# Kernel optimization log

Hardware: AMD Instinct MI355X
Metric: run time of the kernel (lower is better)

The kernel has to match this reference:

```python
import jax, jax.numpy as jnp
import numpy as np

M0, M1 = 16, 8          # scalar / vector multiplicities (16x0e + 8x1o)
NB = 16                  # number_of_basis
RMAX = 8.0               # max_radius
N_NODES, N_EDGES = 10000, 160000
WNUM = M0*M0 + M0*M1 + M1*M1 + M1*M0  # 576, tp weight_numel


def sus(t):
    """e3nn soft_unit_step: exp(-1/t) for t>0 else 0."""
    safe = jnp.where(t > 0, t, 1.0)
    return jnp.where(t > 0, jnp.exp(-1.0 / safe), 0.0)


def setup_inputs():
    key = jax.random.key(0)
    ks = jax.random.split(key, 12)
    D = M0 + 3 * M1  # 40
    x = jax.random.normal(ks[0], (N_NODES, D), jnp.float32)
    edge_index = jax.random.randint(ks[1], (2, N_EDGES), 0, N_NODES, jnp.int32)
    edge_attr = jax.random.normal(ks[2], (N_EDGES, 4), jnp.float32)  # sh lmax=1
    node_attr = jnp.ones((N_NODES, 1), jnp.float32)
    batch = jnp.zeros((N_NODES,), jnp.int32)
    amf = jax.random.uniform(ks[3], (N_EDGES, 1), jnp.float32) * RMAX  # edge lengths
    Wq0 = jax.random.normal(ks[4], (M0, M0), jnp.float32)
    Wq1 = jax.random.normal(ks[5], (M1, M1), jnp.float32)
    Wk1 = jax.random.normal(ks[6], (NB, 16), jnp.float32)
    Wk2 = jax.random.normal(ks[7], (16, WNUM), jnp.float32)
    Wv1 = jax.random.normal(ks[8], (NB, 16), jnp.float32)
    Wv2 = jax.random.normal(ks[9], (16, WNUM), jnp.float32)
    Wd0 = jax.random.normal(ks[10], (M0, M0), jnp.float32)
    Wd1 = jax.random.normal(ks[11], (M1, M1), jnp.float32)
    return dict(x=x, edge_index=edge_index, edge_attr=edge_attr, node_attr=node_attr,
                batch=batch, additional_message_features=amf,
                Wq0=Wq0, Wq1=Wq1, Wk1=Wk1, Wk2=Wk2, Wv1=Wv1, Wv2=Wv2, Wd0=Wd0, Wd1=Wd1)


def reference(x, edge_index, edge_attr, node_attr, batch, additional_message_features,
              Wq0, Wq1, Wk1, Wk2, Wv1, Wv2, Wd0, Wd1):
    n = x.shape[0]
    src, dst = edge_index[0], edge_index[1]
    d = additional_message_features.reshape(-1)  # [E]

    # soft_one_hot_linspace(basis='smooth_finite', cutoff=True) * sqrt(NB)
    centers = jnp.linspace(0.0, RMAX, NB + 2)[1:-1]
    step = RMAX / (NB + 1)
    diff = (d[:, None] - centers) / step
    emb = (1.14136 * np.exp(2.0)) * sus(diff + 1.0) * sus(1.0 - diff) * np.sqrt(NB)  # [E,NB]
    cutoff = sus(10.0 * (1.0 - d / RMAX))  # [E]

    # split irreps: scalars [*,M0], vectors [*,M1,3]
    x0 = x[:, :M0]
    x1 = x[:, M0:].reshape(n, M1, 3)

    # q = Linear(input_irreps -> hidden_irreps): per-irrep linear, 1/sqrt(fan_in)
    q0 = (x0 @ Wq0) / np.sqrt(M0)
    q1 = jnp.einsum('nui,uw->nwi', x1, Wq1) / np.sqrt(M1)

    # radial MLPs producing per-edge tensor-product weights
    def radial(W1, W2):
        h = jax.nn.silu((emb @ W1) / np.sqrt(NB))
        return (h @ W2) / np.sqrt(16.0)  # [E, WNUM]
    wk = radial(Wk1, Wk2)
    wv = radial(Wv1, Wv2)

    xs0, xs1 = x0[src], x1[src]           # gather by edge source
    sh0, sh1 = edge_attr[:, 0], edge_attr[:, 1:4]
    dot11 = jnp.einsum('eui,ei->eu', xs1, sh1) / np.sqrt(3.0)  # 1o x 1o -> 0e CG

    def fctp(w):
        # FullyConnectedTensorProduct(input, sh, out) with per-edge weights.
        s1 = M0 * M0
        s2 = s1 + M0 * M1
        s3 = s2 + M1 * M1
        w1 = w[:, :s1].reshape(-1, M0, M0)   # 0e x 0e -> 0e
        w2 = w[:, s1:s2].reshape(-1, M0, M1) # 0e x 1o -> 1o
        w3 = w[:, s2:s3].reshape(-1, M1, M1) # 1o x 0e -> 1o
        w4 = w[:, s3:].reshape(-1, M1, M0)   # 1o x 1o -> 0e
        norm = 1.0 / np.sqrt(M0 + M1)        # path fan-in normalization
        o0 = (jnp.einsum('euw,eu->ew', w1, xs0 * sh0[:, None]) +
              jnp.einsum('euw,eu->ew', w4, dot11)) * norm            # [E,M0]
        o1 = (jnp.einsum('euw,eu,ei->ewi', w2, xs0, sh1) +
              jnp.einsum('euw,eui->ewi', w3, xs1 * sh0[:, None, None])) * norm  # [E,M1,3]
        return o0, o1

    k0, k1 = fctp(wk)
    v0, v1 = fctp(wv)

    # dot: FullyConnectedTensorProduct(hidden, hidden, '0e') with shared weights
    score = (jnp.einsum('eu,ev,uv->e', q0[dst], k0, Wd0) +
             jnp.einsum('eui,evi,uv->e', q1[dst], k1, Wd1) / np.sqrt(3.0)) / np.sqrt(M0*M0 + M1*M1)

    expv = cutoff * jnp.exp(score)                                   # [E]
    z = jax.ops.segment_sum(expv, dst, num_segments=n)               # [N]
    z = jnp.where(z == 0, 1.0, z)
    alpha = expv / z[dst]
    we = jnp.sqrt(jax.nn.relu(alpha))                                # alpha.relu().sqrt()
    v = jnp.concatenate([v0, v1.reshape(-1, 3 * M1)], axis=1)        # [E,40]
    return jax.ops.segment_sum(we[:, None] * v, dst, num_segments=n) # [N,40]
```

## Files before the change

kernel.cpp:

```cpp
#include <hip/hip_runtime.h>
#include <hip/hip_bf16.h>

#define E_CNT 160000
#define N_CNT 10000

#define INV_STEP   2.125f
#define EMB_C      33.734292f
#define INVS320    0.05590170f
#define INVS8      0.35355339f
#define INV_SQRT3  0.57735027f
#define KSCALE     0.051031036f

#define OFF_FLAG   0
#define OFF_EAF    400016
#define OFF_AMFF   1040016
#define OFF_WK1F   1200656
#define OFF_WV1F   1200912
#define OFF_P      1219600
#define OFF_EXPV   1619600
#define OFF_VBUF   1779600
#define OFF_DEG    8179600
#define OFF_Z      8179600
#define OFF_DEG2   8189600
#define OFF_START  8199600
#define OFF_START2 8209601
#define OFF_CURS   8219602
#define OFF_CURS2  8229602
#define OFF_DPOS   8239602
#define OFF_ELIST2 8399602
#define OFF_G      8559632


static __device__ __forceinline__ float bf2f(__hip_bfloat16 b) { return __bfloat162float(b); }
static __device__ __forceinline__ float sanitize(float v) {
    return fminf(fmaxf(v, -1e30f), 1e30f);
}
static __device__ __forceinline__ unsigned short f2bf(float f) {
    unsigned x = __float_as_uint(f);
    unsigned r = (x + 0x7fffu + ((x >> 16) & 1u)) >> 16;
    return (unsigned short)r;
}
static __device__ __forceinline__ float bflo(unsigned u) { return __uint_as_float(u << 16); }
static __device__ __forceinline__ float bfhi(unsigned u) { return __uint_as_float(u & 0xffff0000u); }
static __device__ __forceinline__ float2 bfp(unsigned u) {
    float2 r; r.x = bflo(u); r.y = bfhi(u); return r;
}

static __device__ __forceinline__ float4 load4(const void* p, int i4, int f32)
{
    if (f32) return ((const float4*)p)[i4];
    uint2 u = ((const uint2*)p)[i4];
    float4 r;
    r.x = bflo(u.x); r.y = bfhi(u.x);
    r.z = bflo(u.y); r.w = bfhi(u.y);
    return r;
}

static __device__ __forceinline__ void ld8(const float* p, float (&r)[8])
{
    float4 a = ((const float4*)p)[0];
    float4 b = ((const float4*)p)[1];
    r[0] = a.x; r[1] = a.y; r[2] = a.z; r[3] = a.w;
    r[4] = b.x; r[5] = b.y; r[6] = b.z; r[7] = b.w;
}
static __device__ __forceinline__ void ld8(const __hip_bfloat16* p, float (&r)[8])
{
    uint4 u = *(const uint4*)p;
    r[0] = bflo(u.x); r[1] = bfhi(u.x); r[2] = bflo(u.y); r[3] = bfhi(u.y);
    r[4] = bflo(u.z); r[5] = bfhi(u.z); r[6] = bflo(u.w); r[7] = bfhi(u.w);
}

__global__ __launch_bounds__(256) void init_kernel(
    const unsigned short* __restrict__ xb, float* __restrict__ ws)
{
    const int idx = blockIdx.x * 256 + threadIdx.x;
    if (idx < 20000) ((int*)(ws + OFF_DEG))[idx] = 0;
    if (blockIdx.x == 0 && threadIdx.x < 64) {
        const int lane = threadIdx.x;
        unsigned e0 = (unsigned)((xb[2 * lane] >> 7) & 0xFF);
        unsigned e1 = (unsigned)((xb[128 + 2 * lane] >> 7) & 0xFF);
        int c = (e0 >= 141 ? 1 : 0) + (e1 >= 141 ? 1 : 0);
#pragma unroll
        for (int off = 1; off < 64; off <<= 1) c += __shfl_xor(c, off);
        if (lane == 0) *(int*)ws = (c >= 8) ? 1 : 0;
    }
}

static __device__ __forceinline__ void do_prep(
    const void* __restrict__ ea, const void* __restrict__ amf,
    const void* __restrict__ Wk1, const void* __restrict__ Wv1,
    const int* __restrict__ ei, float* __restrict__ ws, int i, int f32)
{
    if (i < 160000) ((float4*)(ws + OFF_EAF))[i] = load4(ea, i, f32);
    if (i < 40000) {
        ((float4*)(ws + OFF_AMFF))[i] = load4(amf, i, f32);
#pragma unroll
        for (int k = 0; k < 4; ++k) {
            atomicAdd((int*)(ws + OFF_DEG)  + ei[E_CNT + 4 * i + k], 1);
            atomicAdd((int*)(ws + OFF_DEG2) + ei[4 * i + k], 1);
        }
    }
    if (i < 64) {
        ((float4*)(ws + OFF_WK1F))[i] = load4(Wk1, i, f32);
        ((float4*)(ws + OFF_WV1F))[i] = load4(Wv1, i, f32);
    }
}

template <typename T>
static __device__ __forceinline__ void build_G(
    const T* __restrict__ x, const T* __restrict__ W2b, int n, int p, int c, float* __restrict__ ws)
{
    float xs[40];
#pragma unroll
    for (int q = 0; q < 5; ++q) ld8(x + n * 40 + q * 8, *(float(*)[8])(xs + q * 8));
    const T* W2 = W2b + c * 576;

    float out[96];
#pragma unroll
    for (int k = 0; k < 96; ++k) out[k] = 0.f;

#pragma unroll
    for (int u = 0; u < 16; ++u) {
        float r0[8], r1[8];
        ld8(W2 + u * 16, r0);
        ld8(W2 + u * 16 + 8, r1);
        const float xv = xs[u];
#pragma unroll
        for (int w = 0; w < 8; ++w) {
            out[w]     = fmaf(r0[w], xv, out[w]);
            out[8 + w] = fmaf(r1[w], xv, out[8 + w]);
        }
    }
#pragma unroll
    for (int u = 0; u < 16; ++u) {
        float r[8];
        ld8(W2 + 256 + u * 8, r);
        const float xv = xs[u];
#pragma unroll
        for (int w = 0; w < 8; ++w) out[16 + w] = fmaf(r[w], xv, out[16 + w]);
    }
#pragma unroll
    for (int u = 0; u < 8; ++u) {
        float r[8];
        ld8(W2 + 384 + u * 8, r);
        const float a0 = xs[16 + u * 3 + 0];
        const float a1 = xs[16 + u * 3 + 1];
        const float a2 = xs[16 + u * 3 + 2];
#pragma unroll
        for (int w = 0; w < 8; ++w) {
            out[24 + w * 3 + 0] = fmaf(r[w], a0, out[24 + w * 3 + 0]);
            out[24 + w * 3 + 1] = fmaf(r[w], a1, out[24 + w * 3 + 1]);
            out[24 + w * 3 + 2] = fmaf(r[w], a2, out[24 + w * 3 + 2]);
        }
    }
#pragma unroll
    for (int u = 0; u < 8; ++u) {
        float r0[8], r1[8];
        ld8(W2 + 448 + u * 16, r0);
        ld8(W2 + 448 + u * 16 + 8, r1);
        const float a0 = xs[16 + u * 3 + 0];
        const float a1 = xs[16 + u * 3 + 1];
        const float a2 = xs[16 + u * 3 + 2];
#pragma unroll
        for (int w = 0; w < 8; ++w) {
            out[48 + w * 3 + 0] = fmaf(r0[w], a0, out[48 + w * 3 + 0]);
            out[48 + w * 3 + 1] = fmaf(r0[w], a1, out[48 + w * 3 + 1]);
            out[48 + w * 3 + 2] = fmaf(r0[w], a2, out[48 + w * 3 + 2]);
            out[48 + (8 + w) * 3 + 0] = fmaf(r1[w], a0, out[48 + (8 + w) * 3 + 0]);
            out[48 + (8 + w) * 3 + 1] = fmaf(r1[w], a1, out[48 + (8 + w) * 3 + 1]);
            out[48 + (8 + w) * 3 + 2] = fmaf(r1[w], a2, out[48 + (8 + w) * 3 + 2]);
        }
    }
#pragma unroll
    for (int k = 0; k < 48; ++k) out[48 + k] *= INV_SQRT3;

    uint4 ov[12];
    unsigned* ou = (unsigned*)ov;
#pragma unroll
    for (int k = 0; k < 48; ++k)
        ou[k] = (unsigned)f2bf(out[2 * k]) | ((unsigned)f2bf(out[2 * k + 1]) << 16);
    uint4* gb = (uint4*)(ws + OFF_G) + (size_t)(p * 16 + c) * 120000 + n;
#pragma unroll
    for (int q = 0; q < 12; ++q) gb[q * 10000] = ov[q];
}

template <typename T>
static __device__ __forceinline__ void build_P(
    const T* __restrict__ x, const T* __restrict__ Wq0, const T* __restrict__ Wq1,
    const T* __restrict__ Wd0, const T* __restrict__ Wd1, int n, float* __restrict__ ws)
{
    float xs[40];
#pragma unroll
    for (int q = 0; q < 5; ++q) ld8(x + n * 40 + q * 8, *(float(*)[8])(xs + q * 8));

    float q0[16];
#pragma unroll
    for (int w = 0; w < 16; ++w) q0[w] = 0.f;
#pragma unroll
    for (int u = 0; u < 16; ++u) {
        float r0[8], r1[8];
        ld8(Wq0 + u * 16, r0);
        ld8(Wq0 + u * 16 + 8, r1);
        const float xv = xs[u];
#pragma unroll
        for (int w = 0; w < 8; ++w) {
            q0[w]     = fmaf(r0[w], xv, q0[w]);
            q0[8 + w] = fmaf(r1[w], xv, q0[8 + w]);
        }
    }
#pragma unroll
    for (int w = 0; w < 16; ++w) q0[w] *= 0.25f;

    float p0[16];
#pragma unroll
    for (int v = 0; v < 16; ++v) p0[v] = 0.f;
#pragma unroll
    for (int w = 0; w < 16; ++w) {
        float r0[8], r1[8];
        ld8(Wd0 + w * 16, r0);
        ld8(Wd0 + w * 16 + 8, r1);
        const float qv = q0[w];
#pragma unroll
        for (int v = 0; v < 8; ++v) {
            p0[v]     = fmaf(r0[v], qv, p0[v]);
            p0[8 + v] = fmaf(r1[v], qv, p0[8 + v]);
        }
    }
    float* pn = ws + OFF_P + n * 40;
#pragma unroll
    for (int v = 0; v < 16; ++v) pn[v] = sanitize(p0[v] * INVS320);

    float q1[24];
#pragma unroll
    for (int k = 0; k < 24; ++k) q1[k] = 0.f;
#pragma unroll
    for (int u = 0; u < 8; ++u) {
        float r[8];
        ld8(Wq1 + u * 8, r);
        const float a0 = xs[16 + u * 3 + 0];
        const float a1 = xs[16 + u * 3 + 1];
        const float a2 = xs[16 + u * 3 + 2];
#pragma unroll
        for (int w = 0; w < 8; ++w) {
            q1[w * 3 + 0] = fmaf(r[w], a0, q1[w * 3 + 0]);
            q1[w * 3 + 1] = fmaf(r[w], a1, q1[w * 3 + 1]);
            q1[w * 3 + 2] = fmaf(r[w], a2, q1[w * 3 + 2]);
        }
    }
#pragma unroll
    for (int k = 0; k < 24; ++k) q1[k] *= INVS8;

    float p1[24];
#pragma unroll
    for (int k = 0; k < 24; ++k) p1[k] = 0.f;
#pragma unroll
    for (int w = 0; w < 8; ++w) {
        float r[8];
        ld8(Wd1 + w * 8, r);
        const float b0 = q1[w * 3 + 0];
        const float b1 = q1[w * 3 + 1];
        const float b2 = q1[w * 3 + 2];
#pragma unroll
        for (int v = 0; v < 8; ++v) {
            p1[v * 3 + 0] = fmaf(r[v], b0, p1[v * 3 + 0]);
            p1[v * 3 + 1] = fmaf(r[v], b1, p1[v * 3 + 1]);
            p1[v * 3 + 2] = fmaf(r[v], b2, p1[v * 3 + 2]);
        }
    }
    const float sc = INVS320 * INV_SQRT3;
#pragma unroll
    for (int k = 0; k < 24; ++k) pn[16 + k] = sanitize(p1[k] * sc);
}

__global__ __launch_bounds__(256) void gp_kernel(
    const void* __restrict__ x,
    const void* __restrict__ Wq0, const void* __restrict__ Wq1,
    const void* __restrict__ Wk2, const void* __restrict__ Wv2,
    const void* __restrict__ Wd0, const void* __restrict__ Wd1,
    const void* __restrict__ ea, const void* __restrict__ amf,
    const void* __restrict__ Wk1, const void* __restrict__ Wv1,
    const int* __restrict__ ei,
    float* __restrict__ ws)
{
    const int f32 = *(const int*)ws;
    const int tid = threadIdx.x;
    const int blk = blockIdx.x;
    if (blk < 625) {
        do_prep(ea, amf, Wk1, Wv1, ei, ws, blk * 256 + tid, f32);
        return;
    }
    if (blk < 1875) {
        const int t = (blk - 625) * 256 + tid;
        const int p   = t / 160000;
        const int rem = t - p * 160000;
        const int c   = rem / 10000;
        const int n   = rem - c * 10000;
        const void* W2b = p ? Wv2 : Wk2;
        if (f32) build_G((const float*)x, (const float*)W2b, n, p, c, ws);
        else     build_G((const __hip_bfloat16*)x, (const __hip_bfloat16*)W2b, n, p, c, ws);
        return;
    }
    {
        const int n = (blk - 1875) * 256 + tid;
        if (n >= N_CNT) return;
        if (f32) build_P((const float*)x, (const float*)Wq0, (const float*)Wq1,
                         (const float*)Wd0, (const float*)Wd1, n, ws);
        else     build_P((const __hip_bfloat16*)x, (const __hip_bfloat16*)Wq0,
                         (const __hip_bfloat16*)Wq1, (const __hip_bfloat16*)Wd0,
                         (const __hip_bfloat16*)Wd1, n, ws);
    }
}

__global__ __launch_bounds__(512) void scan_kernel(float* __restrict__ ws)
{
    __shared__ int ssum[512];
    const int t    = threadIdx.x;
    const int half = t >> 8;
    const int lt   = t & 255;
    int* deg   = (int*)(ws + (half ? OFF_DEG2   : OFF_DEG));
    int* start = (int*)(ws + (half ? OFF_START2 : OFF_START));
    int* curs  = (int*)(ws + (half ? OFF_CURS2  : OFF_CURS));
    const int base = lt * 40;
    int s = 0;
    for (int k = 0; k < 40; ++k) {
        int idx = base + k;
        if (idx < N_CNT) s += deg[idx];
    }
    ssum[t] = s;
    __syncthreads();
    for (int off = 1; off < 256; off <<= 1) {
        int v = (lt >= off) ? ssum[t - off] : 0;
        __syncthreads();
        ssum[t] += v;
        __syncthreads();
    }
    int run = ssum[t] - s;
    for (int k = 0; k < 40; ++k) {
        int idx = base + k;
        if (idx < N_CNT) {
            start[idx] = run;
            curs[idx]  = run;
            run += deg[idx];
        }
    }
    if (lt == 255) start[N_CNT] = E_CNT;
    __syncthreads();
    for (int k = t; k < N_CNT; k += 512) ws[OFF_Z + k] = 0.f;
}

__global__ __launch_bounds__(256) void fill_kernel(const int* __restrict__ ei, float* __restrict__ ws)
{
    const int e = blockIdx.x * 256 + threadIdx.x;
    int pd = atomicAdd((int*)(ws + OFF_CURS)  + ei[E_CNT + e], 1);
    int ps = atomicAdd((int*)(ws + OFF_CURS2) + ei[e], 1);
    ((int*)(ws + OFF_ELIST2))[ps] = e;
    ((int*)(ws + OFF_DPOS))[ps]   = pd;
}

static __device__ __forceinline__ void load48p(unsigned (&ub)[48], const uint4* __restrict__ p0)
{
#pragma unroll
    for (int q = 0; q < 12; ++q) {
        uint4 v = p0[(size_t)q * 10000];
        ub[4 * q + 0] = v.x; ub[4 * q + 1] = v.y;
        ub[4 * q + 2] = v.z; ub[4 * q + 3] = v.w;
    }
}

static __device__ __forceinline__ void accum48(const unsigned (&ub)[48], float hc, float sh0,
    float s1x, float s1y, float s1z,
    float (&o0)[16], float (&o1)[24], float (&t2a)[8])
{
    const float hs = hc * sh0;
#define GVAL(k) (((k) & 1) ? bfhi(ub[(k) >> 1]) : bflo(ub[(k) >> 1]))
#pragma unroll
    for (int w = 0; w < 16; ++w) o0[w] = fmaf(hs, GVAL(w), o0[w]);
#pragma unroll
    for (int w = 0; w < 8; ++w) t2a[w] = fmaf(hc, GVAL(16 + w), t2a[w]);
#pragma unroll
    for (int k = 0; k < 24; ++k) o1[k] = fmaf(hs, GVAL(24 + k), o1[k]);
#pragma unroll
    for (int w = 0; w < 16; ++w) {
        float g = GVAL(48 + w * 3 + 0) * s1x;
        g = fmaf(GVAL(48 + w * 3 + 1), s1y, g);
        g = fmaf(GVAL(48 + w * 3 + 2), s1z, g);
        o0[w] = fmaf(hc, g, o0[w]);
    }
#undef GVAL
}

__global__ __launch_bounds__(128, 2) void edge_kernel(
    const int* __restrict__ ei, float* __restrict__ ws)
{
    const int tid  = threadIdx.x;
    const int pass = tid >> 6;
    const int lane = tid & 63;
    const int b  = blockIdx.x;
    const int lb = (b < 2496) ? ((b & 7) * 312 + (b >> 3)) : b;
    const int sidx = lb * 64 + lane;
    const int e    = ((const int*)(ws + OFF_ELIST2))[sidx];
    const int dpos = ((const int*)(ws + OFF_DPOS))[sidx];
    const int src  = ei[e];
    const int dst  = ei[E_CNT + e];

    const uint4* gb = (const uint4*)(ws + OFF_G) + (size_t)pass * 1920000 + src;
    unsigned A[48], B[48];
    load48p(A, gb);
    load48p(B, gb + 120000);

    const float d   = ws[OFF_AMFF + e];
    const float dsv = d * INV_STEP;
    const int i1 = (int)ceilf(dsv) - 1;
    const int i0 = i1 - 1;
    float e0 = 0.f, e1 = 0.f;
    {
        float t1 = dsv - (float)i0;
        float t2 = (float)(i0 + 2) - dsv;
        if (i0 >= 0 && i0 <= 15 && t2 > 0.f)
            e0 = EMB_C * expf(-1.f / t1 - 1.f / t2);
        float u1 = dsv - (float)i1;
        float u2 = (float)(i1 + 2) - dsv;
        if (i1 >= 0 && i1 <= 15 && u1 > 0.f)
            e1 = EMB_C * expf(-1.f / u1 - 1.f / u2);
    }
    const int r0i = (i0 < 0 ? 0 : (i0 > 15 ? 15 : i0)) << 4;
    const int r1i = (i1 < 0 ? 0 : (i1 > 15 ? 15 : i1)) << 4;

    const float* W1 = ws + (pass ? OFF_WV1F : OFF_WK1F);
    float h[16];
#pragma unroll
    for (int j = 0; j < 16; ++j) {
        float s = fmaf(e1, W1[r1i + j], e0 * W1[r0i + j]);
        s *= 0.25f;
        h[j] = s / (1.f + expf(-s));
    }

    const float4 eav = ((const float4*)(ws + OFF_EAF))[e];
    const float sh0 = eav.x, s1x = eav.y, s1y = eav.z, s1z = eav.w;

    float o0[16], o1[24], t2a[8];
#pragma unroll
    for (int i = 0; i < 16; ++i) o0[i] = 0.f;
#pragma unroll
    for (int i = 0; i < 24; ++i) o1[i] = 0.f;
#pragma unroll
    for (int i = 0; i < 8; ++i) t2a[i] = 0.f;

#pragma unroll
    for (int c = 0; c < 16; c += 2) {
        accum48(A, h[c], sh0, s1x, s1y, s1z, o0, o1, t2a);
        if (c + 2 < 16) load48p(A, gb + (size_t)(c + 2) * 120000);
        accum48(B, h[c + 1], sh0, s1x, s1y, s1z, o0, o1, t2a);
        if (c + 3 < 16) load48p(B, gb + (size_t)(c + 3) * 120000);
    }

#pragma unroll
    for (int w = 0; w < 8; ++w) {
        o1[w * 3 + 0] = fmaf(t2a[w], s1x, o1[w * 3 + 0]);
        o1[w * 3 + 1] = fmaf(t2a[w], s1y, o1[w * 3 + 1]);
        o1[w * 3 + 2] = fmaf(t2a[w], s1z, o1[w * 3 + 2]);
    }

    if (pass == 0) {
        const float* pd = ws + OFF_P + dst * 40;
        float sc = 0.f;
#pragma unroll
        for (int j = 0; j < 16; ++j) sc = fmaf(o0[j], pd[j], sc);
#pragma unroll
        for (int j = 0; j < 24; ++j) sc = fmaf(o1[j], pd[16 + j], sc);
        sc = fminf(fmaxf(sc * KSCALE, -60.f), 60.f);
        float ct = 10.f * (1.f - d * 0.125f);
        float cutoff = (ct > 0.f) ? expf(-1.f / ct) : 0.f;
        float ev = fmaxf(cutoff * expf(sc), 0.f);
        ws[OFF_EXPV + dpos] = ev;
        atomicAdd(ws + OFF_Z + dst, ev);
    } else {
        float vo[40];
#pragma unroll
        for (int j = 0; j < 16; ++j) vo[j] = sanitize(o0[j] * KSCALE);
#pragma unroll
        for (int j = 0; j < 24; ++j) vo[16 + j] = sanitize(o1[j] * KSCALE);
        uint4 pk[5];
        unsigned* pu = (unsigned*)pk;
#pragma unroll
        for (int k = 0; k < 20; ++k)
            pu[k] = (unsigned)f2bf(vo[2 * k]) | ((unsigned)f2bf(vo[2 * k + 1]) << 16);
        uint4* vr = (uint4*)((unsigned short*)(ws + OFF_VBUF) + (size_t)dpos * 40);
#pragma unroll
        for (int q = 0; q < 5; ++q) vr[q] = pk[q];
    }
}

__global__ __launch_bounds__(256) void gather_kernel(
    const float* __restrict__ ws, void* __restrict__ out)
{
    const int i = blockIdx.x * 256 + threadIdx.x;
    if (i >= N_CNT * 10) return;
    const int n = i / 10;
    const int q = i - n * 10;
    const int* start = (const int*)(ws + OFF_START);
    const float* expv = ws + OFF_EXPV;
    const unsigned* Vb = (const unsigned*)(ws + OFF_VBUF);
    const int s = start[n], t = start[n + 1];

    float zz = ws[OFF_Z + n];
    const float rz = (zz > 0.f) ? 1.f / zz : 1.f;

    float ax = 0.f, ay = 0.f, az = 0.f, aw = 0.f;
    for (int j = s; j < t; ++j) {
        const float we = sqrtf(fmaxf(expv[j] * rz, 0.f));
        uint2 u = *(const uint2*)(Vb + (size_t)j * 20 + 2 * q);
        float2 v0 = bfp(u.x), v1 = bfp(u.y);
        ax = fmaf(we, v0.x, ax); ay = fmaf(we, v0.y, ay);
        az = fmaf(we, v1.x, az); aw = fmaf(we, v1.y, aw);
    }
    ax = sanitize(ax); ay = sanitize(ay); az = sanitize(az); aw = sanitize(aw);
    const int f32 = *(const int*)ws;
    if (f32) {
        float4 o; o.x = ax; o.y = ay; o.z = az; o.w = aw;
        ((float4*)out)[(size_t)n * 10 + q] = o;
    } else {
        uint2 o;
        o.x = (unsigned)f2bf(ax) | ((unsigned)f2bf(ay) << 16);
        o.y = (unsigned)f2bf(az) | ((unsigned)f2bf(aw) << 16);
        ((uint2*)out)[(size_t)n * 10 + q] = o;
    }
}

extern "C" void kernel_launch(void* const* d_in, const int* in_sizes, int n_in,
                              void* d_out, int out_size, void* d_ws, size_t ws_size,
                              hipStream_t stream)
{
    (void)in_sizes; (void)n_in; (void)out_size; (void)ws_size;
    const void* x   = d_in[0];
    const int*  ei  = (const int*)d_in[1];
    const void* ea  = d_in[2];
    const void* amf = d_in[5];
    const void* Wq0 = d_in[6];
    const void* Wq1 = d_in[7];
    const void* Wk1 = d_in[8];
    const void* Wk2 = d_in[9];
    const void* Wv1 = d_in[10];
    const void* Wv2 = d_in[11];
    const void* Wd0 = d_in[12];
    const void* Wd1 = d_in[13];

    float* ws = (float*)d_ws;

    init_kernel<<<79, 256, 0, stream>>>((const unsigned short*)x, ws);
    gp_kernel<<<1915, 256, 0, stream>>>(x, Wq0, Wq1, Wk2, Wv2, Wd0, Wd1,
                                        ea, amf, Wk1, Wv1, (const int*)ei, ws);
    scan_kernel<<<1, 512, 0, stream>>>(ws);
    fill_kernel<<<625, 256, 0, stream>>>(ei, ws);
    edge_kernel<<<2500, 128, 0, stream>>>(ei, ws);
    gather_kernel<<<(N_CNT * 10 + 255) / 256, 256, 0, stream>>>(ws, d_out);
}
```

Measured before the change: 265.3 us.

## Split each edge's basis reduction across four lanes with shuffle reduction

The edge kernel now assigns four lanes per edge, each handling four of the sixteen radial basis chunks, then reduces the partial outputs with xor shuffles. Grid grows to 5000 blocks of 256 threads, and the block remap is adjusted to match. Output packing and the score/atomic are split across the four lanes. This raises parallelism and memory-level concurrency per edge, but adds 40×2 shuffles per lane and duplicates per-edge setup work (index loads, embedding, h computation) four times.

Result: slower. 341.1 us (+28.6%).

```diff
diff --git a/kernel.cpp b/kernel.cpp
--- a/kernel.cpp
+++ b/kernel.cpp
@@ -389,21 +389,39 @@
 #undef GVAL
 }
 
-__global__ __launch_bounds__(128, 2) void edge_kernel(
+#define PACK8(dstu4, arr, base)                                                  \
+    do {                                                                         \
+        (dstu4).x = (unsigned)f2bf(sanitize((arr)[(base)+0] * KSCALE))           \
+                  | ((unsigned)f2bf(sanitize((arr)[(base)+1] * KSCALE)) << 16);  \
+        (dstu4).y = (unsigned)f2bf(sanitize((arr)[(base)+2] * KSCALE))           \
+                  | ((unsigned)f2bf(sanitize((arr)[(base)+3] * KSCALE)) << 16);  \
+        (dstu4).z = (unsigned)f2bf(sanitize((arr)[(base)+4] * KSCALE))           \
+                  | ((unsigned)f2bf(sanitize((arr)[(base)+5] * KSCALE)) << 16);  \
+        (dstu4).w = (unsigned)f2bf(sanitize((arr)[(base)+6] * KSCALE))           \
+                  | ((unsigned)f2bf(sanitize((arr)[(base)+7] * KSCALE)) << 16);  \
+    } while (0)
+
+__global__ __launch_bounds__(256, 2) void edge_kernel(
     const int* __restrict__ ei, float* __restrict__ ws)
 {
     const int tid  = threadIdx.x;
-    const int pass = tid >> 6;
+    const int wid  = tid >> 6;
+    const int pass = wid & 1;
+    const int halfw = wid >> 1;
     const int lane = tid & 63;
+    const int g    = lane >> 2;
+    const int j    = lane & 3;
+
     const int b  = blockIdx.x;
-    const int lb = (b < 2496) ? ((b & 7) * 312 + (b >> 3)) : b;
-    const int sidx = lb * 64 + lane;
+    const int lb = (b & 7) * 625 + (b >> 3);
+    const int sidx = lb * 32 + halfw * 16 + g;
     const int e    = ((const int*)(ws + OFF_ELIST2))[sidx];
     const int dpos = ((const int*)(ws + OFF_DPOS))[sidx];
     const int src  = ei[e];
     const int dst  = ei[E_CNT + e];
 
-    const uint4* gb = (const uint4*)(ws + OFF_G) + (size_t)pass * 1920000 + src;
+    const uint4* gb = (const uint4*)(ws + OFF_G) + (size_t)pass * 1920000 + src
+                    + (size_t)(4 * j) * 120000;
     unsigned A[48], B[48];
     load48p(A, gb);
     load48p(B, gb + 120000);
@@ -427,12 +445,13 @@
     const int r1i = (i1 < 0 ? 0 : (i1 > 15 ? 15 : i1)) << 4;
 
     const float* W1 = ws + (pass ? OFF_WV1F : OFF_WK1F);
-    float h[16];
-#pragma unroll
-    for (int j = 0; j < 16; ++j) {
-        float s = fmaf(e1, W1[r1i + j], e0 * W1[r0i + j]);
+    float h[4];
+#pragma unroll
+    for (int cc = 0; cc < 4; ++cc) {
+        const int c = 4 * j + cc;
+        float s = fmaf(e1, W1[r1i + c], e0 * W1[r0i + c]);
         s *= 0.25f;
-        h[j] = s / (1.f + expf(-s));
+        h[cc] = s / (1.f + expf(-s));
     }
 
     const float4 eav = ((const float4*)(ws + OFF_EAF))[e];
@@ -446,13 +465,12 @@
 #pragma unroll
     for (int i = 0; i < 8; ++i) t2a[i] = 0.f;
 
-#pragma unroll
-    for (int c = 0; c < 16; c += 2) {
-        accum48(A, h[c], sh0, s1x, s1y, s1z, o0, o1, t2a);
-        if (c + 2 < 16) load48p(A, gb + (size_t)(c + 2) * 120000);
-        accum48(B, h[c + 1], sh0, s1x, s1y, s1z, o0, o1, t2a);
-        if (c + 3 < 16) load48p(B, gb + (size_t)(c + 3) * 120000);
-    }
+    accum48(A, h[0], sh0, s1x, s1y, s1z, o0, o1, t2a);
+    load48p(A, gb + (size_t)2 * 120000);
+    accum48(B, h[1], sh0, s1x, s1y, s1z, o0, o1, t2a);
+    load48p(B, gb + (size_t)3 * 120000);
+    accum48(A, h[2], sh0, s1x, s1y, s1z, o0, o1, t2a);
+    accum48(B, h[3], sh0, s1x, s1y, s1z, o0, o1, t2a);
 
 #pragma unroll
     for (int w = 0; w < 8; ++w) {
@@ -461,33 +479,50 @@
         o1[w * 3 + 2] = fmaf(t2a[w], s1z, o1[w * 3 + 2]);
     }
 
+#pragma unroll
+    for (int k = 0; k < 16; ++k) {
+        float v = o0[k];
+        v += __shfl_xor(v, 1);
+        v += __shfl_xor(v, 2);
+        o0[k] = v;
+    }
+#pragma unroll
+    for (int k = 0; k < 24; ++k) {
+        float v = o1[k];
+        v += __shfl_xor(v, 1);
+        v += __shfl_xor(v, 2);
+        o1[k] = v;
+    }
+
     if (pass == 0) {
-        const float* pd = ws + OFF_P + dst * 40;
-        float sc = 0.f;
-#pragma unroll
-        for (int j = 0; j < 16; ++j) sc = fmaf(o0[j], pd[j], sc);
-#pragma unroll
-        for (int j = 0; j < 24; ++j) sc = fmaf(o1[j], pd[16 + j], sc);
-        sc = fminf(fmaxf(sc * KSCALE, -60.f), 60.f);
-        float ct = 10.f * (1.f - d * 0.125f);
-        float cutoff = (ct > 0.f) ? expf(-1.f / ct) : 0.f;
-        float ev = fmaxf(cutoff * expf(sc), 0.f);
-        ws[OFF_EXPV + dpos] = ev;
-        atomicAdd(ws + OFF_Z + dst, ev);
+        if (j == 0) {
+            const float* pd = ws + OFF_P + dst * 40;
+            float sc = 0.f;
+#pragma unroll
+            for (int k = 0; k < 16; ++k) sc = fmaf(o0[k], pd[k], sc);
+#pragma unroll
+            for (int k = 0; k < 24; ++k) sc = fmaf(o1[k], pd[16 + k], sc);
+            sc = fminf(fmaxf(sc * KSCALE, -60.f), 60.f);
+            float ct = 10.f * (1.f - d * 0.125f);
+            float cutoff = (ct > 0.f) ? expf(-1.f / ct) : 0.f;
+            float ev = fmaxf(cutoff * expf(sc), 0.f);
+            ws[OFF_EXPV + dpos] = ev;
+            atomicAdd(ws + OFF_Z + dst, ev);
+        }
     } else {
-        float vo[40];
-#pragma unroll
-        for (int j = 0; j < 16; ++j) vo[j] = sanitize(o0[j] * KSCALE);
-#pragma unroll
-        for (int j = 0; j < 24; ++j) vo[16 + j] = sanitize(o1[j] * KSCALE);
-        uint4 pk[5];
-        unsigned* pu = (unsigned*)pk;
-#pragma unroll
-        for (int k = 0; k < 20; ++k)
-            pu[k] = (unsigned)f2bf(vo[2 * k]) | ((unsigned)f2bf(vo[2 * k + 1]) << 16);
         uint4* vr = (uint4*)((unsigned short*)(ws + OFF_VBUF) + (size_t)dpos * 40);
-#pragma unroll
-        for (int q = 0; q < 5; ++q) vr[q] = pk[q];
+        uint4 pk;
+        if (j == 0) {
+            PACK8(pk, o0, 0);  vr[0] = pk;
+        } else if (j == 1) {
+            PACK8(pk, o0, 8);  vr[1] = pk;
+            uint4 pk2;
+            PACK8(pk2, o1, 16); vr[4] = pk2;
+        } else if (j == 2) {
+            PACK8(pk, o1, 0);  vr[2] = pk;
+        } else {
+            PACK8(pk, o1, 8);  vr[3] = pk;
+        }
     }
 }
 
@@ -552,6 +587,6 @@
                                         ea, amf, Wk1, Wv1, (const int*)ei, ws);
     scan_kernel<<<1, 512, 0, stream>>>(ws);
     fill_kernel<<<625, 256, 0, stream>>>(ei, ws);
-    edge_kernel<<<2500, 128, 0, stream>>>(ei, ws);
+    edge_kernel<<<5000, 256, 0, stream>>>(ei, ws);
     gather_kernel<<<(N_CNT * 10 + 255) / 256, 256, 0, stream>>>(ws, d_out);
 }
```
